# Kernel tuning notes

Measured on AMD Instinct MI355X. Metric: run time of the kernel, lower is better.

The kernel has to match this reference:

```python
import jax, jax.numpy as jnp
import numpy as np

B, N_CH, T, E = 64, 64, 1000, 512
KS = [3, 5, 7]
TC, AH, GC, HEADS, NCLS = 16, 32, 32, 4, 2
F3 = TC * len(KS)
EPS = 1e-5


def _gat(x, src, dst, W, a_src, a_dst, bias, N):
    # PyG GATConv, concat=False: h = x @ W.T -> [N, H, C]
    H, C = a_src.shape
    h = (x @ W.T).reshape(-1, H, C)
    al_s = (h * a_src).sum(-1)  # [N, H]
    al_d = (h * a_dst).sum(-1)
    e = al_s[src] + al_d[dst]  # [E, H]
    e = jnp.where(e > 0, e, 0.2 * e)  # leaky_relu(0.2)
    emax = jax.ops.segment_max(e, dst, num_segments=N)
    ex = jnp.exp(e - emax[dst])
    denom = jax.ops.segment_sum(ex, dst, num_segments=N)
    alpha = ex / denom[dst]
    out = jax.ops.segment_sum(h[src] * alpha[:, :, None], dst, num_segments=N)
    return out.mean(1) + bias  # concat=False -> head mean, then bias


def _branch(xr, cw, cb, g, b, m, v, w1, b1, w2, b2):
    k = cw.shape[-1]
    o = jax.lax.conv_general_dilated(xr, cw, (1,), [(k // 2, k // 2)],
                                     dimension_numbers=('NCH', 'OIH', 'NCH'))
    o = o + cb[None, :, None]
    o = (o - m[None, :, None]) / jnp.sqrt(v[None, :, None] + EPS) * g[None, :, None] + b[None, :, None]
    o = jax.nn.gelu(o, approximate=False)
    h = jnp.tanh(jnp.einsum('hc,nct->nht', w1, o) + b1[None, :, None])
    s = jnp.einsum('oh,nht->not', w2, h) + b2[None, :, None]  # [N,1,T]
    wts = jax.nn.softmax(s, axis=2)
    return (o * wts).sum(-1)  # [N, TC]


def reference(x, edge_index,
              conv_w_0, conv_b_0, bn_g_0, bn_b_0, bn_m_0, bn_v_0, aw1_0, ab1_0, aw2_0, ab2_0,
              conv_w_1, conv_b_1, bn_g_1, bn_b_1, bn_m_1, bn_v_1, aw1_1, ab1_1, aw2_1, ab2_1,
              conv_w_2, conv_b_2, bn_g_2, bn_b_2, bn_m_2, bn_v_2, aw1_2, ab1_2, aw2_2, ab2_2,
              se_w1, se_b1, se_w2, se_b2,
              gat1_w, gat1_asrc, gat1_adst, gat1_bias, bn1_g, bn1_b, bn1_m, bn1_v,
              skip_w, skip_b,
              gat2_w, gat2_asrc, gat2_adst, gat2_bias, bn2_g, bn2_b, bn2_m, bn2_v,
              fc_w, fc_b):
    Bx, n, Tn = x.shape
    xr = x.reshape(Bx * n, 1, Tn)
    branches = [
        (conv_w_0, conv_b_0, bn_g_0, bn_b_0, bn_m_0, bn_v_0, aw1_0, ab1_0, aw2_0, ab2_0),
        (conv_w_1, conv_b_1, bn_g_1, bn_b_1, bn_m_1, bn_v_1, aw1_1, ab1_1, aw2_1, ab2_1),
        (conv_w_2, conv_b_2, bn_g_2, bn_b_2, bn_m_2, bn_v_2, aw1_2, ab1_2, aw2_2, ab2_2),
    ]
    feats = [_branch(xr, *p) for p in branches]
    xf = jnp.concatenate(feats, axis=1)  # [B*n, F3]
    # SE block (squeeze over all nodes, per original mean over dim 0)
    sq = xf.mean(0, keepdims=True)
    sq = jax.nn.gelu(sq @ se_w1.T + se_b1, approximate=False)
    sq = jax.nn.sigmoid(sq @ se_w2.T + se_b2)
    xf = xf * sq
    # batched edge index + self loops (PyG GATConv default add_self_loops)
    offs = (jnp.arange(Bx) * n).astype(edge_index.dtype)
    src = (edge_index[0][None, :] + offs[:, None]).reshape(-1)
    dst = (edge_index[1][None, :] + offs[:, None]).reshape(-1)
    loops = jnp.arange(Bx * n, dtype=edge_index.dtype)
    src = jnp.concatenate([src, loops])
    dst = jnp.concatenate([dst, loops])
    Nn = Bx * n
    h1 = _gat(xf, src, dst, gat1_w, gat1_asrc, gat1_adst, gat1_bias, Nn)
    h1 = (h1 - bn1_m) / jnp.sqrt(bn1_v + EPS) * bn1_g + bn1_b
    h1 = jax.nn.gelu(h1 + xf @ skip_w.T + skip_b, approximate=False)
    h2 = _gat(h1, src, dst, gat2_w, gat2_asrc, gat2_adst, gat2_bias, Nn)
    h2 = (h2 - bn2_m) / jnp.sqrt(bn2_v + EPS) * bn2_g + bn2_b
    h2 = jax.nn.gelu(h2 + h1, approximate=False)
    pooled = h2.reshape(Bx, n, -1).mean(1)  # global_mean_pool per graph
    return pooled @ fc_w.T + fc_b


def setup_inputs() -> dict:
    key = jax.random.key(0)
    it = iter(jax.random.split(key, 80))
    nk = lambda *s: jax.random.normal(next(it), s, jnp.float32) * 0.1
    d = {}
    d['x'] = jax.random.normal(next(it), (B, N_CH, T), jnp.float32)
    s0 = jax.random.randint(next(it), (E,), 0, N_CH)
    off = jax.random.randint(next(it), (E,), 1, N_CH)
    d['edge_index'] = jnp.stack([s0, (s0 + off) % N_CH]).astype(jnp.int32)  # no self loops
    for i, k in enumerate(KS):
        d[f'conv_w_{i}'] = nk(TC, 1, k); d[f'conv_b_{i}'] = nk(TC)
        d[f'bn_g_{i}'] = 1.0 + nk(TC); d[f'bn_b_{i}'] = nk(TC)
        d[f'bn_m_{i}'] = nk(TC); d[f'bn_v_{i}'] = 1.0 + jnp.abs(nk(TC))
        d[f'aw1_{i}'] = nk(AH, TC); d[f'ab1_{i}'] = nk(AH)
        d[f'aw2_{i}'] = nk(1, AH); d[f'ab2_{i}'] = nk(1)
    d['se_w1'] = nk(F3 // 4, F3); d['se_b1'] = nk(F3 // 4)
    d['se_w2'] = nk(F3, F3 // 4); d['se_b2'] = nk(F3)
    d['gat1_w'] = nk(HEADS * GC, F3)
    d['gat1_asrc'] = nk(HEADS, GC); d['gat1_adst'] = nk(HEADS, GC); d['gat1_bias'] = nk(GC)
    d['bn1_g'] = 1.0 + nk(GC); d['bn1_b'] = nk(GC); d['bn1_m'] = nk(GC); d['bn1_v'] = 1.0 + jnp.abs(nk(GC))
    d['skip_w'] = nk(GC, F3); d['skip_b'] = nk(GC)
    d['gat2_w'] = nk(HEADS * GC, GC)
    d['gat2_asrc'] = nk(HEADS, GC); d['gat2_adst'] = nk(HEADS, GC); d['gat2_bias'] = nk(GC)
    d['bn2_g'] = 1.0 + nk(GC); d['bn2_b'] = nk(GC); d['bn2_m'] = nk(GC); d['bn2_v'] = 1.0 + jnp.abs(nk(GC))
    d['fc_w'] = nk(NCLS, GC); d['fc_b'] = nk(NCLS)
    return d
```

## Files before the change

### kernel.cpp

```cpp
#include <hip/hip_runtime.h>
#include <math.h>

#define N_NODES 4096
#define T_LEN 1000
#define TCH 16
#define AHD 32
#define F3D 48
#define GCD 32
#define NPG 64
#define NGRAPH 64
#define BN_EPS 1e-5f

typedef _Float16 half4_t __attribute__((ext_vector_type(4)));
typedef float float4_t __attribute__((ext_vector_type(4)));

__device__ __forceinline__ float fast_rcp(float x){ return __builtin_amdgcn_rcpf(x); }
__device__ __forceinline__ float gelu_exact(float v){
    return 0.5f*v*(1.0f+erff(v*0.70710678118654752f));
}

struct BranchParams {
    const float* conv_w; const float* conv_b;
    const float* bn_g; const float* bn_b; const float* bn_m; const float* bn_v;
    const float* aw1; const float* ab1; const float* aw2; const float* ab2;
    int K; int col0;
};

__global__ __launch_bounds__(256)
void branch_kernel(const float* __restrict__ x,
                   BranchParams bp0, BranchParams bp1, BranchParams bp2,
                   float* __restrict__ xf)
{
    __shared__ __align__(16) float xs_f[1056];
    __shared__ __align__(8)  _Float16 xsc[4][1048];
    __shared__ __align__(8)  _Float16 cws16[256];
    __shared__ float s_arr[1024];
    __shared__ __align__(16) float shiftc[16];
    __shared__ float scl[16];
    __shared__ float redm[4], reds[4];
    __shared__ __align__(16) float fredw[4][16];

    const BranchParams bp = (blockIdx.y==0)? bp0 : (blockIdx.y==1)? bp1 : bp2;
    const int tid = threadIdx.x;
    const int node = blockIdx.x;
    const int K = bp.K;
    const float* xrow = x + (size_t)node*T_LEN;

    for (int j=tid;j<1056;j+=256){
        int q = j-8;
        xs_f[j] = (q>=0 && q<T_LEN)? xrow[q] : 0.f;
    }
    if (tid<16){
        float s = bp.bn_g[tid]*rsqrtf(bp.bn_v[tid]+BN_EPS);
        scl[tid]=s;
        shiftc[tid] = (bp.conv_b[tid]-bp.bn_m[tid])*s + bp.bn_b[tid];
    }
    __syncthreads();
    for (int j=tid;j<1048;j+=256){
        xsc[0][j]=(_Float16)xs_f[j];
        xsc[1][j]=(_Float16)xs_f[j+1];
        xsc[2][j]=(_Float16)xs_f[j+2];
        xsc[3][j]=(_Float16)xs_f[j+3];
    }
    {
        int ch=tid>>4, tap=tid&15;
        cws16[tid] = (tap<K)? (_Float16)(bp.conv_w[ch*K+tap]*scl[ch]) : (_Float16)0.f;
    }
    __syncthreads();

    const int lane = tid&63, wave = tid>>6;
    const int col  = lane&15;
    const int kg   = (lane>>4)<<2;

    const half4_t  acw = *(const half4_t*)&cws16[col*16+kg];
    const float4_t csh = *(const float4_t*)&shiftc[kg];

    const float TWO_LOG2E = 2.8853900817779268f;

    float4_t wr0 = *(const float4_t*)&bp.aw1[(size_t)col*TCH + kg];
    float4_t wr1 = *(const float4_t*)&bp.aw1[(size_t)(col+16)*TCH + kg];
    half4_t a0,a1;
    #pragma unroll
    for (int r=0;r<4;r++){ a0[r]=(_Float16)(wr0[r]*TWO_LOG2E); a1[r]=(_Float16)(wr1[r]*TWO_LOG2E); }
    float4_t c0  = *(const float4_t*)&bp.ab1[kg];
    float4_t c1  = *(const float4_t*)&bp.ab1[16+kg];
    #pragma unroll
    for (int r=0;r<4;r++){ c0[r]*=TWO_LOG2E; c1[r]*=TWO_LOG2E; }
    const float4_t w20 = *(const float4_t*)&bp.aw2[kg];
    const float4_t w21 = *(const float4_t*)&bp.aw2[16+kg];
    const float b2v = bp.ab2[0];
    const float w2sum8 = w20[0]+w20[1]+w20[2]+w20[3]+w21[0]+w21[1]+w21[2]+w21[3];

    const float C1GE = -2.30220818f;
    const float C2GE = -0.10294324f;

    const int abase = 8 + wave*256 + col + kg - K/2;
    const int sh = abase & 3;
    const _Float16* xw_base = &xsc[sh][abase - sh];

    half4_t oreg[16];
    #pragma unroll
    for (int i=0;i<16;i++){
        half4_t xw = *(const half4_t*)(xw_base + i*16);
        float4_t d = __builtin_amdgcn_mfma_f32_16x16x16f16(acw, xw, csh, 0,0,0);

        float vv[4], dd[4];
        #pragma unroll
        for (int r=0;r<4;r++){
            float v = d[r];
            vv[r] = v;
            float t = fmaxf(v, -9.0f);
            float u = t*t;
            float pq = fmaf(C2GE, u, C1GE);
            dd[r] = __builtin_amdgcn_exp2f(pq*t) + 1.0f;
        }
        half4_t ob;
        {
            float rp0 = fast_rcp(dd[0]*dd[1]);
            float rp1 = fast_rcp(dd[2]*dd[3]);
            ob[0] = (_Float16)(vv[0]*(dd[1]*rp0));
            ob[1] = (_Float16)(vv[1]*(dd[0]*rp0));
            ob[2] = (_Float16)(vv[2]*(dd[3]*rp1));
            ob[3] = (_Float16)(vv[3]*(dd[2]*rp1));
        }
        oreg[i] = ob;

        float4_t h0 = __builtin_amdgcn_mfma_f32_16x16x16f16(a0, ob, c0, 0,0,0);
        float4_t h1 = __builtin_amdgcn_mfma_f32_16x16x16f16(a1, ob, c1, 0,0,0);
        float accr = 0.f;
        #pragma unroll
        for (int r=0;r<4;r++){
            float e0 = __builtin_amdgcn_exp2f(h0[r]) + 1.0f;
            float e1 = __builtin_amdgcn_exp2f(h1[r]) + 1.0f;
            float rp = fast_rcp(e0*e1);
            accr = fmaf(w20[r], e1*rp, accr);
            accr = fmaf(w21[r], e0*rp, accr);
        }
        float part = fmaf(-2.0f, accr, w2sum8);
        part += __shfl_xor(part,16);
        part += __shfl_xor(part,32);
        const int pos0 = wave*256 + i*16;
        if (lane<16) s_arr[pos0+lane] = (pos0+lane < T_LEN)? (part + b2v) : -INFINITY;
    }
    __syncthreads();

    float sv[4];
    #pragma unroll
    for (int ii=0;ii<4;ii++) sv[ii]=s_arr[tid+ii*256];
    float m = fmaxf(fmaxf(sv[0],sv[1]),fmaxf(sv[2],sv[3]));
    #pragma unroll
    for (int off=32;off;off>>=1) m = fmaxf(m, __shfl_xor(m,off));
    if (lane==0) redm[wave]=m;
    __syncthreads();
    const float bm = fmaxf(fmaxf(redm[0],redm[1]),fmaxf(redm[2],redm[3]));
    float e[4]; float ls=0.f;
    #pragma unroll
    for (int ii=0;ii<4;ii++){ e[ii]=__expf(sv[ii]-bm); ls+=e[ii]; }
    #pragma unroll
    for (int off=32;off;off>>=1) ls += __shfl_xor(ls,off);
    if (lane==0) reds[wave]=ls;
    __syncthreads();
    const float invS = fast_rcp(reds[0]+reds[1]+reds[2]+reds[3]);
    #pragma unroll
    for (int ii=0;ii<4;ii++) s_arr[tid+ii*256]=e[ii];
    __syncthreads();

    float4_t acc = {0.f,0.f,0.f,0.f};
    #pragma unroll
    for (int i=0;i<16;i++){
        float ev = s_arr[wave*256 + i*16 + col];
        half4_t ob = oreg[i];
        #pragma unroll
        for (int r=0;r<4;r++) acc[r] += (float)ob[r]*ev;
    }
    #pragma unroll
    for (int off=1;off<16;off<<=1){
        #pragma unroll
        for (int r=0;r<4;r++) acc[r] += __shfl_xor(acc[r], off);
    }
    if (col==0) *(float4_t*)&fredw[wave][kg] = acc;
    __syncthreads();
    if (tid<16){
        float v = (fredw[0][tid]+fredw[1][tid]+fredw[2][tid]+fredw[3][tid])*invS;
        xf[(size_t)node*F3D + bp.col0 + tid] = v;
    }
}

__global__ __launch_bounds__(256)
void colsum_kernel(const float* __restrict__ xf, float* __restrict__ colmean){
    int col = blockIdx.x;
    int tid = threadIdx.x;
    float s=0.f;
    for (int i=tid;i<N_NODES;i+=256) s += xf[(size_t)i*F3D+col];
    #pragma unroll
    for (int off=32;off;off>>=1) s += __shfl_xor(s,off);
    __shared__ float red[4];
    if ((tid&63)==0) red[tid>>6]=s;
    __syncthreads();
    if (tid==0) colmean[col] = (red[0]+red[1]+red[2]+red[3])*(1.0f/(float)N_NODES);
}

__global__ __launch_bounds__(64)
void gate_kernel(const float* __restrict__ colmean,
                 const float* __restrict__ se_w1, const float* __restrict__ se_b1,
                 const float* __restrict__ se_w2, const float* __restrict__ se_b2,
                 float* __restrict__ gate){
    __shared__ float sq[F3D];
    __shared__ float g1[12];
    int tid=threadIdx.x;
    if (tid<F3D) sq[tid]=colmean[tid];
    __syncthreads();
    if (tid<12){
        float v=se_b1[tid];
        for (int j=0;j<F3D;j++) v += se_w1[tid*F3D+j]*sq[j];
        g1[tid]=gelu_exact(v);
    }
    __syncthreads();
    if (tid<F3D){
        float v=se_b2[tid];
        for (int m2=0;m2<12;m2++) v += se_w2[tid*12+m2]*g1[m2];
        gate[tid] = fast_rcp(1.0f+__expf(-v));
    }
}

__device__ __forceinline__ void edge_decode(const int* __restrict__ ei, int epg,
                                            int e, int be, int& src, int& dst){
    if (e < be){ int b=e/epg, j=e-b*epg; src=ei[j]+b*NPG; dst=ei[epg+j]+b*NPG; }
    else { src=dst=e-be; }
}

__global__ __launch_bounds__(256)
void edge_count(const int* __restrict__ ei, int epg, int* __restrict__ deg){
    int e = blockIdx.x*256+threadIdx.x;
    int be = NGRAPH*epg, total = be + N_NODES;
    if (e>=total) return;
    int s,d; edge_decode(ei,epg,e,be,s,d);
    atomicAdd(&deg[d],1);
}

__global__ __launch_bounds__(1024)
void scan_kernel(const int* __restrict__ deg, int* __restrict__ rowstart,
                 int* __restrict__ cursor){
    __shared__ int part[1024];
    int tid=threadIdx.x;
    int v0=deg[tid*4],v1=deg[tid*4+1],v2=deg[tid*4+2],v3=deg[tid*4+3];
    part[tid]=v0+v1+v2+v3;
    __syncthreads();
    for (int off=1;off<1024;off<<=1){
        int t=(tid>=off)?part[tid-off]:0;
        __syncthreads();
        part[tid]+=t;
        __syncthreads();
    }
    int base=(tid>0)?part[tid-1]:0;
    int r0=base, r1=r0+v0, r2=r1+v1, r3=r2+v2;
    rowstart[tid*4]=r0; rowstart[tid*4+1]=r1; rowstart[tid*4+2]=r2; rowstart[tid*4+3]=r3;
    cursor[tid*4]=r0;   cursor[tid*4+1]=r1;   cursor[tid*4+2]=r2;   cursor[tid*4+3]=r3;
    if (tid==1023) rowstart[4096]=part[1023];
}

__global__ __launch_bounds__(256)
void edge_fill(const int* __restrict__ ei, int epg, int* __restrict__ cursor,
               int* __restrict__ cols){
    int e = blockIdx.x*256+threadIdx.x;
    int be = NGRAPH*epg, total = be + N_NODES;
    if (e>=total) return;
    int s,d; edge_decode(ei,epg,e,be,s,d);
    int pos = atomicAdd(&cursor[d],1);
    cols[pos]=s;
}

__global__ __launch_bounds__(128)
void gat_h1_kernel(const float* __restrict__ xin_g, const float* __restrict__ gate,
                   const float* __restrict__ W,
                   const float* __restrict__ a_src, const float* __restrict__ a_dst,
                   float* __restrict__ hbuf, float* __restrict__ als, float* __restrict__ ald){
    __shared__ float xin[F3D];
    __shared__ float hs[128];
    int node=blockIdx.x, tid=threadIdx.x;
    if (tid<F3D) xin[tid]=xin_g[(size_t)node*F3D+tid]*gate[tid];
    __syncthreads();
    float acc=0.f;
    const float* wr = W + (size_t)tid*F3D;
    #pragma unroll
    for (int j=0;j<F3D;j++) acc += wr[j]*xin[j];
    hs[tid]=acc;
    hbuf[(size_t)node*128+tid]=acc;
    __syncthreads();
    if (tid<8){
        int head=tid&3;
        const float* av = (tid<4)? a_src : a_dst;
        float s=0.f;
        for (int c=0;c<GCD;c++) s += hs[head*GCD+c]*av[head*GCD+c];
        if (tid<4) als[(size_t)node*4+head]=s;
        else       ald[(size_t)node*4+head]=s;
    }
}

__global__ __launch_bounds__(512)
void gat_tail_kernel(const int* __restrict__ rowstart, const int* __restrict__ cols,
                     const float* __restrict__ als, const float* __restrict__ ald,
                     const float* __restrict__ hbuf,
                     const float* __restrict__ bias1,
                     const float* __restrict__ bn1_g, const float* __restrict__ bn1_b,
                     const float* __restrict__ bn1_m, const float* __restrict__ bn1_v,
                     const float* __restrict__ xf, const float* __restrict__ gate,
                     const float* __restrict__ skip_w, const float* __restrict__ skip_b,
                     const float* __restrict__ W2,
                     const float* __restrict__ asrc2, const float* __restrict__ adst2,
                     const float* __restrict__ bias2,
                     const float* __restrict__ bn2_g, const float* __restrict__ bn2_b,
                     const float* __restrict__ bn2_m, const float* __restrict__ bn2_v,
                     const float* __restrict__ fc_w, const float* __restrict__ fc_b,
                     float* __restrict__ out)
{
    __shared__ float hb[64*128];
    __shared__ float xh[64*48];
    __shared__ float h1l[64*32];
    __shared__ float a1s[256], a1d[256], a2s[256], a2d[256];
    __shared__ float skw[32*48];
    __shared__ float poolv[32];

    const int g = blockIdx.x;
    const int tid = threadIdx.x;
    const int n0 = g*NPG;

    for (int i=tid;i<64*128;i+=512) hb[i] = hbuf[(size_t)n0*128 + i];
    for (int i=tid;i<64*48;i+=512)  xh[i] = xf[(size_t)n0*F3D + i] * gate[i%F3D];
    for (int i=tid;i<32*48;i+=512)  skw[i] = skip_w[i];
    if (tid<256){ a1s[tid]=als[n0*4+tid]; a1d[tid]=ald[n0*4+tid]; }
    __syncthreads();

    for (int p=0;p<4;p++){
        const int nl = p*16 + (tid>>5);
        const int c  = tid&31;
        const float4 ad = *(const float4*)&a1d[nl*4];
        float m0=0,m1=0,m2=0,m3=0,d0=0,d1=0,d2=0,d3=0;
        const int s0=rowstart[n0+nl], s1=rowstart[n0+nl+1];
        for (int e=s0;e<s1;e++){
            const int sl = cols[e]-n0;
            const float4 as=*(const float4*)&a1s[sl*4];
            float e0=as.x+ad.x; e0=e0>0.f?e0:0.2f*e0; float w0=__expf(e0);
            float e1=as.y+ad.y; e1=e1>0.f?e1:0.2f*e1; float w1=__expf(e1);
            float e2=as.z+ad.z; e2=e2>0.f?e2:0.2f*e2; float w2=__expf(e2);
            float e3=as.w+ad.w; e3=e3>0.f?e3:0.2f*e3; float w3=__expf(e3);
            const float* hr=&hb[sl*128];
            m0+=w0*hr[c]; m1+=w1*hr[32+c]; m2+=w2*hr[64+c]; m3+=w3*hr[96+c];
            d0+=w0; d1+=w1; d2+=w2; d3+=w3;
        }
        float acc = 0.25f*(m0*fast_rcp(d0)+m1*fast_rcp(d1)+m2*fast_rcp(d2)+m3*fast_rcp(d3)) + bias1[c];
        acc = (acc-bn1_m[c])*rsqrtf(bn1_v[c]+BN_EPS)*bn1_g[c]+bn1_b[c];
        float sk = skip_b[c];
        const float* xr=&xh[nl*F3D];
        #pragma unroll
        for (int j=0;j<F3D;j++) sk += xr[j]*skw[c*F3D+j];
        h1l[nl*32+c]=gelu_exact(acc+sk);
    }
    __syncthreads();

    for (int i=tid;i<64*128;i+=512){
        const int nl=i>>7, r=i&127;
        const float4* h1r=(const float4*)&h1l[nl*32];
        const float4* wr =(const float4*)&W2[r*32];
        float acc=0.f;
        #pragma unroll
        for (int j=0;j<8;j++){
            float4 a=h1r[j], b=wr[j];
            acc += a.x*b.x + a.y*b.y + a.z*b.z + a.w*b.w;
        }
        hb[i]=acc;
    }
    __syncthreads();

    {
        const int which = tid>>8;
        const int idx = tid&255;
        const int nl=idx>>2, h=idx&3;
        const float* av = which? &adst2[h*32] : &asrc2[h*32];
        const float* hr = &hb[nl*128 + h*32];
        float s=0.f;
        #pragma unroll
        for (int c=0;c<32;c++) s += hr[c]*av[c];
        if (which) a2d[idx]=s; else a2s[idx]=s;
    }
    __syncthreads();

    for (int p=0;p<4;p++){
        const int nl = p*16 + (tid>>5);
        const int c  = tid&31;
        const float4 ad = *(const float4*)&a2d[nl*4];
        float m0=0,m1=0,m2=0,m3=0,d0=0,d1=0,d2=0,d3=0;
        const int s0=rowstart[n0+nl], s1=rowstart[n0+nl+1];
        for (int e=s0;e<s1;e++){
            const int sl = cols[e]-n0;
            const float4 as=*(const float4*)&a2s[sl*4];
            float e0=as.x+ad.x; e0=e0>0.f?e0:0.2f*e0; float w0=__expf(e0);
            float e1=as.y+ad.y; e1=e1>0.f?e1:0.2f*e1; float w1=__expf(e1);
            float e2=as.z+ad.z; e2=e2>0.f?e2:0.2f*e2; float w2=__expf(e2);
            float e3=as.w+ad.w; e3=e3>0.f?e3:0.2f*e3; float w3=__expf(e3);
            const float* hr=&hb[sl*128];
            m0+=w0*hr[c]; m1+=w1*hr[32+c]; m2+=w2*hr[64+c]; m3+=w3*hr[96+c];
            d0+=w0; d1+=w1; d2+=w2; d3+=w3;
        }
        float acc = 0.25f*(m0*fast_rcp(d0)+m1*fast_rcp(d1)+m2*fast_rcp(d2)+m3*fast_rcp(d3)) + bias2[c];
        acc = (acc-bn2_m[c])*rsqrtf(bn2_v[c]+BN_EPS)*bn2_g[c]+bn2_b[c];
        float v = acc + h1l[nl*32+c];
        xh[nl*32+c]=gelu_exact(v);
    }
    __syncthreads();

    if (tid<32){
        float s=0.f;
        for (int n=0;n<NPG;n++) s += xh[n*32+tid];
        poolv[tid]=s*(1.0f/(float)NPG);
    }
    __syncthreads();
    if (tid<2){
        float o=fc_b[tid];
        #pragma unroll
        for (int c=0;c<GCD;c++) o += poolv[c]*fc_w[tid*GCD+c];
        out[g*2+tid]=o;
    }
}

extern "C" void kernel_launch(void* const* d_in, const int* in_sizes, int n_in,
                              void* d_out, int out_size, void* d_ws, size_t ws_size,
                              hipStream_t stream){
    const float* x = (const float*)d_in[0];
    const int* ei = (const int*)d_in[1];
    const int epg = in_sizes[1]/2;

    float* ws = (float*)d_ws;
    float* xf      = ws;
    float* colmean = xf + (size_t)N_NODES*F3D;
    float* gate    = colmean + 64;
    float* hbuf    = gate + 64;
    float* als     = hbuf + (size_t)N_NODES*128;
    float* ald     = als + (size_t)N_NODES*4;
    int*   deg      = (int*)(ald + (size_t)N_NODES*4);
    int*   rowstart = deg + N_NODES;
    int*   cursor   = rowstart + N_NODES + 1;
    int*   cols     = cursor + N_NODES;

    auto P = [&](int i){ return (const float*)d_in[i]; };

    const int etot = NGRAPH*epg + N_NODES;
    hipMemsetAsync(deg, 0, (size_t)N_NODES*sizeof(int), stream);
    edge_count<<<(etot+255)/256,256,0,stream>>>(ei,epg,deg);
    scan_kernel<<<1,1024,0,stream>>>(deg,rowstart,cursor);
    edge_fill<<<(etot+255)/256,256,0,stream>>>(ei,epg,cursor,cols);

    BranchParams bps[3];
    const int Ks[3] = {3,5,7};
    for (int b=0;b<3;b++){
        int base = 2 + b*10;
        bps[b].conv_w = P(base+0); bps[b].conv_b = P(base+1);
        bps[b].bn_g = P(base+2);   bps[b].bn_b = P(base+3);
        bps[b].bn_m = P(base+4);   bps[b].bn_v = P(base+5);
        bps[b].aw1 = P(base+6);    bps[b].ab1 = P(base+7);
        bps[b].aw2 = P(base+8);    bps[b].ab2 = P(base+9);
        bps[b].K = Ks[b]; bps[b].col0 = b*TCH;
    }
    branch_kernel<<<dim3(N_NODES,3),256,0,stream>>>(x, bps[0], bps[1], bps[2], xf);

    colsum_kernel<<<F3D,256,0,stream>>>(xf,colmean);
    gate_kernel<<<1,64,0,stream>>>(colmean,P(32),P(33),P(34),P(35),gate);

    gat_h1_kernel<<<N_NODES,128,0,stream>>>(xf,gate,P(36),P(37),P(38),hbuf,als,ald);

    gat_tail_kernel<<<NGRAPH,512,0,stream>>>(
        rowstart,cols,als,ald,hbuf,
        P(39),P(40),P(41),P(42),P(43),
        xf,gate,P(44),P(45),
        P(46),P(47),P(48),P(49),P(50),P(51),P(52),P(53),
        P(54),P(55),(float*)d_out);
}
```

Baseline: 252.1 us.

## Fuse colsum/gate into neighbors, build per-graph local CSR, drop softmax max pass

Accumulates column sums with atomics inside the branch kernel and recomputes the SE gate inside the GAT kernels, removing the colsum and gate launches. Replaces the global degree count/scan/fill CSR build with one small block that builds a 64-node local CSR reused by all graphs. Removes the softmax max reduction and a barrier by folding log2e into the score weights and using exp2 directly. Risks include atomic contention on 48 addresses, redundant gate recomputation per block, and possible overflow without max subtraction.

```diff
diff --git a/kernel.cpp b/kernel.cpp
--- a/kernel.cpp
+++ b/kernel.cpp
@@ -29,7 +29,7 @@
 __global__ __launch_bounds__(256)
 void branch_kernel(const float* __restrict__ x,
                    BranchParams bp0, BranchParams bp1, BranchParams bp2,
-                   float* __restrict__ xf)
+                   float* __restrict__ xf, float* __restrict__ colacc)
 {
     __shared__ __align__(16) float xs_f[1056];
     __shared__ __align__(8)  _Float16 xsc[4][1048];
@@ -37,7 +37,7 @@
     __shared__ float s_arr[1024];
     __shared__ __align__(16) float shiftc[16];
     __shared__ float scl[16];
-    __shared__ float redm[4], reds[4];
+    __shared__ float reds[4];
     __shared__ __align__(16) float fredw[4][16];
 
     const BranchParams bp = (blockIdx.y==0)? bp0 : (blockIdx.y==1)? bp1 : bp2;
@@ -76,6 +76,7 @@
     const float4_t csh = *(const float4_t*)&shiftc[kg];
 
     const float TWO_LOG2E = 2.8853900817779268f;
+    const float LOG2E = 1.4426950408889634f;
 
     float4_t wr0 = *(const float4_t*)&bp.aw1[(size_t)col*TCH + kg];
     float4_t wr1 = *(const float4_t*)&bp.aw1[(size_t)(col+16)*TCH + kg];
@@ -86,9 +87,11 @@
     float4_t c1  = *(const float4_t*)&bp.ab1[16+kg];
     #pragma unroll
     for (int r=0;r<4;r++){ c0[r]*=TWO_LOG2E; c1[r]*=TWO_LOG2E; }
-    const float4_t w20 = *(const float4_t*)&bp.aw2[kg];
-    const float4_t w21 = *(const float4_t*)&bp.aw2[16+kg];
-    const float b2v = bp.ab2[0];
+    float4_t w20 = *(const float4_t*)&bp.aw2[kg];
+    float4_t w21 = *(const float4_t*)&bp.aw2[16+kg];
+    #pragma unroll
+    for (int r=0;r<4;r++){ w20[r]*=LOG2E; w21[r]*=LOG2E; }
+    const float b2v = bp.ab2[0]*LOG2E;
     const float w2sum8 = w20[0]+w20[1]+w20[2]+w20[3]+w21[0]+w21[1]+w21[2]+w21[3];
 
     const float C1GE = -2.30220818f;
@@ -147,15 +150,9 @@
     float sv[4];
     #pragma unroll
     for (int ii=0;ii<4;ii++) sv[ii]=s_arr[tid+ii*256];
-    float m = fmaxf(fmaxf(sv[0],sv[1]),fmaxf(sv[2],sv[3]));
-    #pragma unroll
-    for (int off=32;off;off>>=1) m = fmaxf(m, __shfl_xor(m,off));
-    if (lane==0) redm[wave]=m;
-    __syncthreads();
-    const float bm = fmaxf(fmaxf(redm[0],redm[1]),fmaxf(redm[2],redm[3]));
     float e[4]; float ls=0.f;
     #pragma unroll
-    for (int ii=0;ii<4;ii++){ e[ii]=__expf(sv[ii]-bm); ls+=e[ii]; }
+    for (int ii=0;ii<4;ii++){ e[ii]=__builtin_amdgcn_exp2f(sv[ii]); ls+=e[ii]; }
     #pragma unroll
     for (int off=32;off;off>>=1) ls += __shfl_xor(ls,off);
     if (lane==0) reds[wave]=ls;
@@ -183,102 +180,70 @@
     if (tid<16){
         float v = (fredw[0][tid]+fredw[1][tid]+fredw[2][tid]+fredw[3][tid])*invS;
         xf[(size_t)node*F3D + bp.col0 + tid] = v;
-    }
-}
-
-__global__ __launch_bounds__(256)
-void colsum_kernel(const float* __restrict__ xf, float* __restrict__ colmean){
-    int col = blockIdx.x;
-    int tid = threadIdx.x;
-    float s=0.f;
-    for (int i=tid;i<N_NODES;i+=256) s += xf[(size_t)i*F3D+col];
-    #pragma unroll
-    for (int off=32;off;off>>=1) s += __shfl_xor(s,off);
-    __shared__ float red[4];
-    if ((tid&63)==0) red[tid>>6]=s;
-    __syncthreads();
-    if (tid==0) colmean[col] = (red[0]+red[1]+red[2]+red[3])*(1.0f/(float)N_NODES);
-}
-
-__global__ __launch_bounds__(64)
-void gate_kernel(const float* __restrict__ colmean,
-                 const float* __restrict__ se_w1, const float* __restrict__ se_b1,
-                 const float* __restrict__ se_w2, const float* __restrict__ se_b2,
-                 float* __restrict__ gate){
-    __shared__ float sq[F3D];
+        atomicAdd(&colacc[bp.col0 + tid], v);
+    }
+}
+
+__global__ __launch_bounds__(128)
+void csr_local_kernel(const int* __restrict__ ei, int epg,
+                      int* __restrict__ rowstart, int* __restrict__ cols){
+    __shared__ int deg[64], cur[64], rs[65];
+    const int tid = threadIdx.x;
+    if (tid<64) deg[tid]=0;
+    __syncthreads();
+    const int total = epg + 64;
+    for (int e=tid;e<total;e+=128){
+        int d = (e<epg)? ei[epg+e] : (e-epg);
+        atomicAdd(&deg[d],1);
+    }
+    __syncthreads();
+    if (tid<64){
+        int v = deg[tid];
+        int s = v;
+        #pragma unroll
+        for (int off=1;off<64;off<<=1){
+            int t = __shfl_up(s, off);
+            if (tid >= off) s += t;
+        }
+        rs[tid+1] = s;
+        if (tid==0) rs[0]=0;
+        cur[tid] = s - v;
+    }
+    __syncthreads();
+    for (int e=tid;e<total;e+=128){
+        int sN,dN;
+        if (e<epg){ sN=ei[e]; dN=ei[epg+e]; } else { sN=dN=e-epg; }
+        int pos = atomicAdd(&cur[dN],1);
+        cols[pos]=sN;
+    }
+    if (tid<65) rowstart[tid]=rs[tid];
+}
+
+__global__ __launch_bounds__(128)
+void gat_h1_kernel(const float* __restrict__ xf, const float* __restrict__ colacc,
+                   const float* __restrict__ se_w1, const float* __restrict__ se_b1,
+                   const float* __restrict__ se_w2, const float* __restrict__ se_b2,
+                   const float* __restrict__ W,
+                   const float* __restrict__ a_src, const float* __restrict__ a_dst,
+                   float* __restrict__ hbuf, float* __restrict__ als, float* __restrict__ ald){
+    __shared__ float cm[F3D];
     __shared__ float g1[12];
-    int tid=threadIdx.x;
-    if (tid<F3D) sq[tid]=colmean[tid];
+    __shared__ float xin[F3D];
+    __shared__ float hs[128];
+    const int node=blockIdx.x, tid=threadIdx.x;
+    if (tid<F3D) cm[tid]=colacc[tid]*(1.0f/(float)N_NODES);
     __syncthreads();
     if (tid<12){
         float v=se_b1[tid];
-        for (int j=0;j<F3D;j++) v += se_w1[tid*F3D+j]*sq[j];
+        for (int j=0;j<F3D;j++) v += se_w1[tid*F3D+j]*cm[j];
         g1[tid]=gelu_exact(v);
     }
     __syncthreads();
     if (tid<F3D){
         float v=se_b2[tid];
         for (int m2=0;m2<12;m2++) v += se_w2[tid*12+m2]*g1[m2];
-        gate[tid] = fast_rcp(1.0f+__expf(-v));
-    }
-}
-
-__device__ __forceinline__ void edge_decode(const int* __restrict__ ei, int epg,
-                                            int e, int be, int& src, int& dst){
-    if (e < be){ int b=e/epg, j=e-b*epg; src=ei[j]+b*NPG; dst=ei[epg+j]+b*NPG; }
-    else { src=dst=e-be; }
-}
-
-__global__ __launch_bounds__(256)
-void edge_count(const int* __restrict__ ei, int epg, int* __restrict__ deg){
-    int e = blockIdx.x*256+threadIdx.x;
-    int be = NGRAPH*epg, total = be + N_NODES;
-    if (e>=total) return;
-    int s,d; edge_decode(ei,epg,e,be,s,d);
-    atomicAdd(&deg[d],1);
-}
-
-__global__ __launch_bounds__(1024)
-void scan_kernel(const int* __restrict__ deg, int* __restrict__ rowstart,
-                 int* __restrict__ cursor){
-    __shared__ int part[1024];
-    int tid=threadIdx.x;
-    int v0=deg[tid*4],v1=deg[tid*4+1],v2=deg[tid*4+2],v3=deg[tid*4+3];
-    part[tid]=v0+v1+v2+v3;
-    __syncthreads();
-    for (int off=1;off<1024;off<<=1){
-        int t=(tid>=off)?part[tid-off]:0;
-        __syncthreads();
-        part[tid]+=t;
-        __syncthreads();
-    }
-    int base=(tid>0)?part[tid-1]:0;
-    int r0=base, r1=r0+v0, r2=r1+v1, r3=r2+v2;
-    rowstart[tid*4]=r0; rowstart[tid*4+1]=r1; rowstart[tid*4+2]=r2; rowstart[tid*4+3]=r3;
-    cursor[tid*4]=r0;   cursor[tid*4+1]=r1;   cursor[tid*4+2]=r2;   cursor[tid*4+3]=r3;
-    if (tid==1023) rowstart[4096]=part[1023];
-}
-
-__global__ __launch_bounds__(256)
-void edge_fill(const int* __restrict__ ei, int epg, int* __restrict__ cursor,
-               int* __restrict__ cols){
-    int e = blockIdx.x*256+threadIdx.x;
-    int be = NGRAPH*epg, total = be + N_NODES;
-    if (e>=total) return;
-    int s,d; edge_decode(ei,epg,e,be,s,d);
-    int pos = atomicAdd(&cursor[d],1);
-    cols[pos]=s;
-}
-
-__global__ __launch_bounds__(128)
-void gat_h1_kernel(const float* __restrict__ xin_g, const float* __restrict__ gate,
-                   const float* __restrict__ W,
-                   const float* __restrict__ a_src, const float* __restrict__ a_dst,
-                   float* __restrict__ hbuf, float* __restrict__ als, float* __restrict__ ald){
-    __shared__ float xin[F3D];
-    __shared__ float hs[128];
-    int node=blockIdx.x, tid=threadIdx.x;
-    if (tid<F3D) xin[tid]=xin_g[(size_t)node*F3D+tid]*gate[tid];
+        xin[tid] = xf[(size_t)node*F3D+tid]*fast_rcp(1.0f+__expf(-v));
+    }
     __syncthreads();
     float acc=0.f;
     const float* wr = W + (size_t)tid*F3D;
@@ -304,7 +269,9 @@
                      const float* __restrict__ bias1,
                      const float* __restrict__ bn1_g, const float* __restrict__ bn1_b,
                      const float* __restrict__ bn1_m, const float* __restrict__ bn1_v,
-                     const float* __restrict__ xf, const float* __restrict__ gate,
+                     const float* __restrict__ xf, const float* __restrict__ colacc,
+                     const float* __restrict__ se_w1, const float* __restrict__ se_b1,
+                     const float* __restrict__ se_w2, const float* __restrict__ se_b2,
                      const float* __restrict__ skip_w, const float* __restrict__ skip_b,
                      const float* __restrict__ W2,
                      const float* __restrict__ asrc2, const float* __restrict__ adst2,
@@ -320,13 +287,29 @@
     __shared__ float a1s[256], a1d[256], a2s[256], a2d[256];
     __shared__ float skw[32*48];
     __shared__ float poolv[32];
+    __shared__ float cm[F3D], g1[12], gate_sh[F3D];
 
     const int g = blockIdx.x;
     const int tid = threadIdx.x;
     const int n0 = g*NPG;
 
+    if (tid<F3D) cm[tid]=colacc[tid]*(1.0f/(float)N_NODES);
+    __syncthreads();
+    if (tid<12){
+        float v=se_b1[tid];
+        for (int j=0;j<F3D;j++) v += se_w1[tid*F3D+j]*cm[j];
+        g1[tid]=gelu_exact(v);
+    }
+    __syncthreads();
+    if (tid<F3D){
+        float v=se_b2[tid];
+        for (int m2=0;m2<12;m2++) v += se_w2[tid*12+m2]*g1[m2];
+        gate_sh[tid]=fast_rcp(1.0f+__expf(-v));
+    }
+    __syncthreads();
+
     for (int i=tid;i<64*128;i+=512) hb[i] = hbuf[(size_t)n0*128 + i];
-    for (int i=tid;i<64*48;i+=512)  xh[i] = xf[(size_t)n0*F3D + i] * gate[i%F3D];
+    for (int i=tid;i<64*48;i+=512)  xh[i] = xf[(size_t)n0*F3D + i] * gate_sh[i%F3D];
     for (int i=tid;i<32*48;i+=512)  skw[i] = skip_w[i];
     if (tid<256){ a1s[tid]=als[n0*4+tid]; a1d[tid]=ald[n0*4+tid]; }
     __syncthreads();
@@ -336,9 +319,9 @@
         const int c  = tid&31;
         const float4 ad = *(const float4*)&a1d[nl*4];
         float m0=0,m1=0,m2=0,m3=0,d0=0,d1=0,d2=0,d3=0;
-        const int s0=rowstart[n0+nl], s1=rowstart[n0+nl+1];
+        const int s0=rowstart[nl], s1=rowstart[nl+1];
         for (int e=s0;e<s1;e++){
-            const int sl = cols[e]-n0;
+            const int sl = cols[e];
             const float4 as=*(const float4*)&a1s[sl*4];
             float e0=as.x+ad.x; e0=e0>0.f?e0:0.2f*e0; float w0=__expf(e0);
             float e1=as.y+ad.y; e1=e1>0.f?e1:0.2f*e1; float w1=__expf(e1);
@@ -390,9 +373,9 @@
         const int c  = tid&31;
         const float4 ad = *(const float4*)&a2d[nl*4];
         float m0=0,m1=0,m2=0,m3=0,d0=0,d1=0,d2=0,d3=0;
-        const int s0=rowstart[n0+nl], s1=rowstart[n0+nl+1];
+        const int s0=rowstart[nl], s1=rowstart[nl+1];
         for (int e=s0;e<s1;e++){
-            const int sl = cols[e]-n0;
+            const int sl = cols[e];
             const float4 as=*(const float4*)&a2s[sl*4];
             float e0=as.x+ad.x; e0=e0>0.f?e0:0.2f*e0; float w0=__expf(e0);
             float e1=as.y+ad.y; e1=e1>0.f?e1:0.2f*e1; float w1=__expf(e1);
@@ -432,23 +415,17 @@
 
     float* ws = (float*)d_ws;
     float* xf      = ws;
-    float* colmean = xf + (size_t)N_NODES*F3D;
-    float* gate    = colmean + 64;
-    float* hbuf    = gate + 64;
+    float* colacc  = xf + (size_t)N_NODES*F3D;
+    float* hbuf    = colacc + 64;
     float* als     = hbuf + (size_t)N_NODES*128;
     float* ald     = als + (size_t)N_NODES*4;
-    int*   deg      = (int*)(ald + (size_t)N_NODES*4);
-    int*   rowstart = deg + N_NODES;
-    int*   cursor   = rowstart + N_NODES + 1;
-    int*   cols     = cursor + N_NODES;
+    int*   rowstart = (int*)(ald + (size_t)N_NODES*4);
+    int*   cols     = rowstart + 80;
 
     auto P = [&](int i){ return (const float*)d_in[i]; };
 
-    const int etot = NGRAPH*epg + N_NODES;
-    hipMemsetAsync(deg, 0, (size_t)N_NODES*sizeof(int), stream);
-    edge_count<<<(etot+255)/256,256,0,stream>>>(ei,epg,deg);
-    scan_kernel<<<1,1024,0,stream>>>(deg,rowstart,cursor);
-    edge_fill<<<(etot+255)/256,256,0,stream>>>(ei,epg,cursor,cols);
+    hipMemsetAsync(colacc, 0, 64*sizeof(float), stream);
+    csr_local_kernel<<<1,128,0,stream>>>(ei,epg,rowstart,cols);
 
     BranchParams bps[3];
     const int Ks[3] = {3,5,7};
@@ -461,17 +438,16 @@
         bps[b].aw2 = P(base+8);    bps[b].ab2 = P(base+9);
         bps[b].K = Ks[b]; bps[b].col0 = b*TCH;
     }
-    branch_kernel<<<dim3(N_NODES,3),256,0,stream>>>(x, bps[0], bps[1], bps[2], xf);
-
-    colsum_kernel<<<F3D,256,0,stream>>>(xf,colmean);
-    gate_kernel<<<1,64,0,stream>>>(colmean,P(32),P(33),P(34),P(35),gate);
-
-    gat_h1_kernel<<<N_NODES,128,0,stream>>>(xf,gate,P(36),P(37),P(38),hbuf,als,ald);
+    branch_kernel<<<dim3(N_NODES,3),256,0,stream>>>(x, bps[0], bps[1], bps[2], xf, colacc);
+
+    gat_h1_kernel<<<N_NODES,128,0,stream>>>(xf,colacc,P(32),P(33),P(34),P(35),
+                                            P(36),P(37),P(38),hbuf,als,ald);
 
     gat_tail_kernel<<<NGRAPH,512,0,stream>>>(
         rowstart,cols,als,ald,hbuf,
         P(39),P(40),P(41),P(42),P(43),
-        xf,gate,P(44),P(45),
+        xf,colacc,P(32),P(33),P(34),P(35),
+        P(44),P(45),
         P(46),P(47),P(48),P(49),P(50),P(51),P(52),P(53),
         P(54),P(55),(float*)d_out);
 }
```

New measurement: 238.8 us. 5.3% less time.
